# Kernel tuning notes

Measured on AMD Instinct MI355X. Metric: run time of the kernel, lower is better.

Reference implementation:

```python
import math
import jax, jax.numpy as jnp
import numpy as np

BS, N, D, H = 4, 512, 1024, 16
HD = D // H


def setup_inputs() -> dict:
    key = jax.random.key(0)
    ks = jax.random.split(key, 12)
    s = 1.0 / math.sqrt(D)
    return {
        "x": jax.random.normal(ks[0], (BS, N, D), jnp.float32),
        "r": jax.random.normal(ks[1], (BS, 3, N, N), jnp.float32),
        "bias": jax.random.normal(ks[2], (BS, H, N, N), jnp.float32),
        "mask": jax.random.randint(ks[3], (BS, 1, N, N), 0, 2, jnp.int32),
        "wq": jax.random.normal(ks[4], (D, D), jnp.float32) * s,
        "bq": jnp.zeros((D,), jnp.float32),
        "wk": jax.random.normal(ks[5], (D, D), jnp.float32) * s,
        "bk": jnp.zeros((D,), jnp.float32),
        "wv": jax.random.normal(ks[6], (D, D), jnp.float32) * s,
        "bv": jnp.zeros((D,), jnp.float32),
        "wo": jax.random.normal(ks[7], (D, 1), jnp.float32) * s,
        "bo": jnp.zeros((1,), jnp.float32),
    }


def reference(x, r, bias, mask, wq, bq, wk, bk, wv, bv, wo, bo):
    bs, n, d = x.shape
    # projections -> (bs, h, n, hd)
    q = (x @ wq + bq).reshape(bs, n, H, HD).transpose(0, 2, 1, 3)
    k = (x @ wk + bk).reshape(bs, n, H, HD).transpose(0, 2, 1, 3)
    v = (x @ wv + bv).reshape(bs, n, H, HD).transpose(0, 2, 1, 3)
    logits = jnp.einsum("bhid,bhjd->bhij", q, k) / math.sqrt(HD) + bias
    logits = jnp.where(mask == 0, jnp.float32(-1e9), logits)
    w = jax.nn.softmax(logits, axis=-1)  # (bs,h,n,n)
    # o[b,i,c,h,d] = sum_j r[b,c,i,j] * w[b,h,i,j] * v[b,h,j,d]
    o = jnp.einsum("bcij,bhij,bhjd->bichd", r, w, v)
    o = o.reshape(bs, n, 3, d)
    force = o @ wo + bo  # (bs, n, 3, 1)
    return force
```

## Files before the change

kernel.cpp:

```cpp
#include <hip/hip_runtime.h>
#include <stdint.h>

#define BSZ 4
#define NSEQ 512
#define DMOD 1024
#define NH 16
#define HD 64

typedef __attribute__((ext_vector_type(8))) short bf16x8;
typedef __attribute__((ext_vector_type(4))) float f32x4;

__device__ __forceinline__ unsigned short f2bf(float f) {
    union { float f; uint32_t u; } v; v.f = f;
    uint32_t u = v.u;
    u += 0x7FFFu + ((u >> 16) & 1u);
    return (unsigned short)(u >> 16);
}

__device__ __forceinline__ void gload_lds16(const unsigned short* g, unsigned short* l) {
    __builtin_amdgcn_global_load_lds(
        (const __attribute__((address_space(1))) void*)g,
        (__attribute__((address_space(3))) void*)l, 16, 0, 0);
}

__global__ __launch_bounds__(256) void k_prep(
        const float* __restrict__ x, const float* __restrict__ wq, const float* __restrict__ wk,
        const float* __restrict__ wv, const float* __restrict__ bv, const float* __restrict__ wo,
        unsigned short* __restrict__ xb, unsigned short* __restrict__ wqt,
        unsigned short* __restrict__ wkt, float* __restrict__ wv2t, float* __restrict__ bv2) {
    __shared__ float t[32][33];
    int bx = blockIdx.x, tid = threadIdx.x;
    if (bx < 2048) {
        int i = bx * 256 + tid;
        float4 v = ((const float4*)x)[i];
        ushort4 o; o.x = f2bf(v.x); o.y = f2bf(v.y); o.z = f2bf(v.z); o.w = f2bf(v.w);
        ((ushort4*)xb)[i] = o;
    } else if (bx < 4096) {
        int g = bx - 2048; int z = g >> 10; g &= 1023;
        const float* src = z ? wk : wq;
        unsigned short* dst = z ? wkt : wqt;
        int be = (g & 31) * 32, bc = (g >> 5) * 32;
        int tx = tid & 31, ty = tid >> 5;
        #pragma unroll
        for (int yy = 0; yy < 32; yy += 8)
            t[ty + yy][tx] = src[(size_t)(be + ty + yy) * DMOD + bc + tx];
        __syncthreads();
        #pragma unroll
        for (int yy = 0; yy < 32; yy += 8)
            dst[(size_t)(bc + ty + yy) * DMOD + be + tx] = f2bf(t[tx][ty + yy]);
    } else {
        int g = bx - 4096;
        int grp = tid >> 6, l = tid & 63;
        int e = g * 4 + grp;
        float out = 0.f;
        #pragma unroll
        for (int it = 0; it < 16; ++it) {
            float v = wv[(size_t)e * DMOD + it * 64 + l] * wo[it * 64 + l];
            #pragma unroll
            for (int off = 1; off < 64; off <<= 1) v += __shfl_xor(v, off, 64);
            if (l == it) out = v;
        }
        if (l < 16) wv2t[l * DMOD + e] = out;
        if (g == 0 && grp == 0) {
            float ob = 0.f;
            #pragma unroll
            for (int it = 0; it < 16; ++it) {
                float v = bv[it * 64 + l] * wo[it * 64 + l];
                #pragma unroll
                for (int off = 1; off < 64; off <<= 1) v += __shfl_xor(v, off, 64);
                if (l == it) ob = v;
            }
            if (l < 16) bv2[l] = ob;
        }
    }
}

__global__ __launch_bounds__(256, 3) void k_mid(
        const float* __restrict__ x, const float* __restrict__ wv2t, const float* __restrict__ bv2,
        const unsigned short* __restrict__ xb, const unsigned short* __restrict__ wqt,
        const unsigned short* __restrict__ wkt, const float* __restrict__ bq,
        const float* __restrict__ bk, float* __restrict__ u,
        unsigned short* __restrict__ qT, unsigned short* __restrict__ kT) {
    __shared__ unsigned short lA[128 * 64];
    __shared__ unsigned short lB[128 * 64];
    int bx = blockIdx.x, tid = threadIdx.x;
    if (bx >= 256) {
        int wave = (bx - 256) * 4 + (tid >> 6);
        int l = tid & 63;
        int b = wave >> 9, j = wave & 511;
        const float* xr = x + (size_t)(b * NSEQ + j) * DMOD;
        float p[16];
        #pragma unroll
        for (int h = 0; h < 16; ++h) p[h] = 0.f;
        for (int it = 0; it < 16; ++it) {
            int e = l + it * 64;
            float xv = xr[e];
            #pragma unroll
            for (int h = 0; h < 16; ++h) p[h] += xv * wv2t[h * DMOD + e];
        }
        #pragma unroll
        for (int h = 0; h < 16; ++h) {
            #pragma unroll
            for (int off = 1; off < 64; off <<= 1) p[h] += __shfl_xor(p[h], off, 64);
        }
        float out = 0.f;
        #pragma unroll
        for (int h = 0; h < 16; ++h) if (l == h) out = p[h] + bv2[h];
        if (l < 16) u[(b * 16 + l) * NSEQ + j] = out;
        return;
    }
    int g = bx;
    int mt = g & 15, nt8 = (g >> 4) & 7, z = g >> 7;
    const unsigned short* Wt = z ? wkt : wqt;
    const float* bias = z ? bk : bq;
    unsigned short* outT = z ? kT : qT;
    float scale = z ? 1.f : 0.125f;
    int m0 = mt * 128, n0 = nt8 * 128;
    int w = tid >> 6, lane = tid & 63;
    int wr = w >> 1, wc = w & 1;
    int quad = lane >> 4, cs = lane & 15;
    int l8 = lane >> 3, l7 = lane & 7;
    int sg = l7 ^ l8;

    f32x4 acc[4][4];
    #pragma unroll
    for (int mi = 0; mi < 4; ++mi)
        #pragma unroll
        for (int ni = 0; ni < 4; ++ni) acc[mi][ni] = (f32x4){0.f, 0.f, 0.f, 0.f};

    for (int kc = 0; kc < 16; ++kc) {
        int k0 = kc * 64;
        #pragma unroll
        for (int q = 0; q < 4; ++q) {
            int row = w * 32 + q * 8 + l8;
            gload_lds16(xb + (size_t)(m0 + row) * DMOD + k0 + sg * 8,
                        &lA[(w * 32 + q * 8) * 64]);
            gload_lds16(Wt + (size_t)(n0 + row) * DMOD + k0 + sg * 8,
                        &lB[(w * 32 + q * 8) * 64]);
        }
        __syncthreads();
        #pragma unroll
        for (int ks = 0; ks < 2; ++ks) {
            bf16x8 af[4], bfr[4];
            #pragma unroll
            for (int mi = 0; mi < 4; ++mi) {
                int row = wr * 64 + mi * 16 + cs;
                int gq = (ks * 4 + quad) ^ (row & 7);
                af[mi] = *(const bf16x8*)&lA[row * 64 + gq * 8];
            }
            #pragma unroll
            for (int ni = 0; ni < 4; ++ni) {
                int row = wc * 64 + ni * 16 + cs;
                int gq = (ks * 4 + quad) ^ (row & 7);
                bfr[ni] = *(const bf16x8*)&lB[row * 64 + gq * 8];
            }
            #pragma unroll
            for (int mi = 0; mi < 4; ++mi)
                #pragma unroll
                for (int ni = 0; ni < 4; ++ni)
                    acc[mi][ni] = __builtin_amdgcn_mfma_f32_16x16x32_bf16(
                        af[mi], bfr[ni], acc[mi][ni], 0, 0, 0);
        }
        __syncthreads();
    }
    #pragma unroll
    for (int ni = 0; ni < 4; ++ni) {
        int n = n0 + wc * 64 + ni * 16 + cs;
        int h = n >> 6, d = n & 63;
        float bvv = bias[n];
        #pragma unroll
        for (int mi = 0; mi < 4; ++mi) {
            #pragma unroll
            for (int rr = 0; rr < 4; ++rr) {
                int mg = m0 + wr * 64 + mi * 16 + quad * 4 + rr;
                int b = mg >> 9, i = mg & 511;
                outT[(size_t)((b * 16 + h) * NSEQ + i) * HD + d] =
                    f2bf((acc[mi][ni][rr] + bvv) * scale);
            }
        }
    }
}

__global__ __launch_bounds__(512, 4) void k_attn(
        const unsigned short* __restrict__ qT, const unsigned short* __restrict__ kT,
        const float* __restrict__ bias, const int* __restrict__ mask,
        const float* __restrict__ u, const float* __restrict__ r,
        float* __restrict__ spart, float* __restrict__ P) {
    __shared__ float rT4[16 * 64 * 4];
    int tid = threadIdx.x;
    int w = tid >> 6, lane = tid & 63;
    int quad = lane >> 4, col = lane & 15;
    int it = blockIdx.x, jc = blockIdx.y, bz = blockIdx.z;
    int b = bz >> 1, hg = bz & 1;
    int i0 = it * 16, j0 = jc * 64;
    int h = hg * 8 + w;
    int bh = b * 16 + h;

    float sr0[2], sr1[2], sr2[2], smf[2];
    const float* rbase = r + (size_t)b * 3 * NSEQ * NSEQ;
    const int* mrow = mask + (size_t)b * NSEQ * NSEQ;
    #pragma unroll
    for (int t = 0; t < 2; ++t) {
        int slot = t * 512 + tid;
        int il = slot >> 6, jl = slot & 63;
        size_t off = (size_t)(i0 + il) * NSEQ + j0 + jl;
        sr0[t] = rbase[off];
        sr1[t] = rbase[(size_t)NSEQ * NSEQ + off];
        sr2[t] = rbase[2 * (size_t)NSEQ * NSEQ + off];
        smf[t] = (float)mrow[off];
    }

    const unsigned short* qbase = qT + ((size_t)(bh * NSEQ + i0 + col)) * HD + quad * 8;
    bf16x8 a0 = *(const bf16x8*)qbase;
    bf16x8 a1 = *(const bf16x8*)(qbase + 32);

    bf16x8 kf0[4], kf1[4];
    #pragma unroll
    for (int jt = 0; jt < 4; ++jt) {
        const unsigned short* kbase = kT + ((size_t)(bh * NSEQ + j0 + jt * 16 + col)) * HD + quad * 8;
        kf0[jt] = *(const bf16x8*)kbase;
        kf1[jt] = *(const bf16x8*)(kbase + 32);
    }
    const float* brow = bias + (size_t)bh * NSEQ * NSEQ;
    float bvv[16];
    #pragma unroll
    for (int jt = 0; jt < 4; ++jt) {
        int j = j0 + jt * 16 + col;
        #pragma unroll
        for (int rr = 0; rr < 4; ++rr) {
            int i = i0 + quad * 4 + rr;
            bvv[jt * 4 + rr] = __builtin_nontemporal_load(&brow[(size_t)i * NSEQ + j]);
        }
    }
    const float* ub = u + (size_t)bh * NSEQ;
    float uvv[4];
    #pragma unroll
    for (int jt = 0; jt < 4; ++jt) uvv[jt] = ub[j0 + jt * 16 + col];

    #pragma unroll
    for (int t = 0; t < 2; ++t) {
        int slot = t * 512 + tid;
        float4 pk; pk.x = sr0[t]; pk.y = sr1[t]; pk.z = sr2[t]; pk.w = smf[t];
        *(float4*)&rT4[slot * 4] = pk;
    }

    asm volatile("s_waitcnt lgkmcnt(0)" ::: "memory");
    __builtin_amdgcn_sched_barrier(0);
    __builtin_amdgcn_s_barrier();
    __builtin_amdgcn_sched_barrier(0);

    float sp[4] = {0.f, 0.f, 0.f, 0.f};
    float pc0[4] = {0.f, 0.f, 0.f, 0.f};
    float pc1[4] = {0.f, 0.f, 0.f, 0.f};
    float pc2[4] = {0.f, 0.f, 0.f, 0.f};
    #pragma unroll
    for (int jt = 0; jt < 4; ++jt) {
        f32x4 acc = (f32x4){0.f, 0.f, 0.f, 0.f};
        acc = __builtin_amdgcn_mfma_f32_16x16x32_bf16(a0, kf0[jt], acc, 0, 0, 0);
        acc = __builtin_amdgcn_mfma_f32_16x16x32_bf16(a1, kf1[jt], acc, 0, 0, 0);
        float uv = uvv[jt];
        int jl = jt * 16 + col;
        #pragma unroll
        for (int rr = 0; rr < 4; ++rr) {
            int il = quad * 4 + rr;
            float4 v = *(const float4*)&rT4[(il * 64 + jl) * 4];
            float lg = acc[rr] + bvv[jt * 4 + rr];
            float e = __expf(lg) * v.w;
            sp[rr] += e;
            float eu = e * uv;
            pc0[rr] += eu * v.x;
            pc1[rr] += eu * v.y;
            pc2[rr] += eu * v.z;
        }
    }
    #pragma unroll
    for (int rr = 0; rr < 4; ++rr) {
        #pragma unroll
        for (int off = 1; off < 16; off <<= 1) {
            sp[rr]  += __shfl_xor(sp[rr], off, 64);
            pc0[rr] += __shfl_xor(pc0[rr], off, 64);
            pc1[rr] += __shfl_xor(pc1[rr], off, 64);
            pc2[rr] += __shfl_xor(pc2[rr], off, 64);
        }
    }
    if (col == 0) {
        #pragma unroll
        for (int rr = 0; rr < 4; ++rr) {
            int il = quad * 4 + rr;
            spart[((size_t)bh * NSEQ + i0 + il) * 8 + jc] = sp[rr];
            size_t pb = ((((size_t)bh * 32 + it) * 16 + il) * 8 + jc) * 3;
            P[pb + 0] = pc0[rr];
            P[pb + 1] = pc1[rr];
            P[pb + 2] = pc2[rr];
        }
    }
}

__global__ __launch_bounds__(256) void k_final(
        const float* __restrict__ spart, const float* __restrict__ P,
        const float* __restrict__ bo, float* __restrict__ out) {
    __shared__ float part[4][16][3];
    int bx = blockIdx.x;
    int b = bx >> 5, it = bx & 31;
    int tid = threadIdx.x;
    int il = tid & 15, h = tid >> 4;
    int w = tid >> 6;
    int bh = b * 16 + h;
    int i = it * 16 + il;
    const float* sprow = spart + ((size_t)bh * NSEQ + i) * 8;
    float4 sa = *(const float4*)sprow;
    float4 sb = *(const float4*)(sprow + 4);
    float s = sa.x + sa.y + sa.z + sa.w + sb.x + sb.y + sb.z + sb.w;
    float sinv = (s > 0.f) ? 1.f / s : 0.f;
    const float* pbase = P + (((size_t)bh * 32 + it) * 16 + il) * 24;
    float f[3] = {0.f, 0.f, 0.f};
    #pragma unroll
    for (int q = 0; q < 6; ++q) {
        float4 v = *(const float4*)(pbase + q * 4);
        f[(q * 4 + 0) % 3] += v.x;
        f[(q * 4 + 1) % 3] += v.y;
        f[(q * 4 + 2) % 3] += v.z;
        f[(q * 4 + 3) % 3] += v.w;
    }
    f[0] *= sinv; f[1] *= sinv; f[2] *= sinv;
    #pragma unroll
    for (int c = 0; c < 3; ++c) {
        f[c] += __shfl_xor(f[c], 16, 64);
        f[c] += __shfl_xor(f[c], 32, 64);
    }
    if ((tid & 48) == 0) {
        part[w][il][0] = f[0]; part[w][il][1] = f[1]; part[w][il][2] = f[2];
    }
    __syncthreads();
    if (tid < 16) {
        float bov = bo[0];
        float o0 = part[0][tid][0] + part[1][tid][0] + part[2][tid][0] + part[3][tid][0];
        float o1 = part[0][tid][1] + part[1][tid][1] + part[2][tid][1] + part[3][tid][1];
        float o2 = part[0][tid][2] + part[1][tid][2] + part[2][tid][2] + part[3][tid][2];
        size_t row = (size_t)b * NSEQ + it * 16 + tid;
        out[row * 3 + 0] = o0 + bov;
        out[row * 3 + 1] = o1 + bov;
        out[row * 3 + 2] = o2 + bov;
    }
}

extern "C" void kernel_launch(void* const* d_in, const int* in_sizes, int n_in,
                              void* d_out, int out_size, void* d_ws, size_t ws_size,
                              hipStream_t stream) {
    const float* x    = (const float*)d_in[0];
    const float* rr   = (const float*)d_in[1];
    const float* bias = (const float*)d_in[2];
    const int*   mask = (const int*)d_in[3];
    const float* wq   = (const float*)d_in[4];
    const float* bq   = (const float*)d_in[5];
    const float* wk   = (const float*)d_in[6];
    const float* bk   = (const float*)d_in[7];
    const float* wv   = (const float*)d_in[8];
    const float* bv   = (const float*)d_in[9];
    const float* wo   = (const float*)d_in[10];
    const float* bo   = (const float*)d_in[11];
    float* out = (float*)d_out;

    char* ws = (char*)d_ws;
    unsigned short* xb    = (unsigned short*)(ws + 0);
    unsigned short* wqt   = (unsigned short*)(ws + 4194304);
    unsigned short* wkt   = (unsigned short*)(ws + 6291456);
    float*          wv2t  = (float*)(ws + 8388608);
    float*          bv2   = (float*)(ws + 8454144);
    float*          u     = (float*)(ws + 8454400);
    unsigned short* qT    = (unsigned short*)(ws + 8585472);
    unsigned short* kT    = (unsigned short*)(ws + 12779776);
    float*          spart = (float*)(ws + 16974080);
    float*          P     = (float*)(ws + 18022656);

    k_prep<<<4352, 256, 0, stream>>>(x, wq, wk, wv, bv, wo, xb, wqt, wkt, wv2t, bv2);
    k_mid<<<768, 256, 0, stream>>>(x, wv2t, bv2, xb, wqt, wkt, bq, bk, u, qT, kT);
    k_attn<<<dim3(32, 8, 8), 512, 0, stream>>>(qT, kT, bias, mask, u, rr, spart, P);
    k_final<<<128, 256, 0, stream>>>(spart, P, bo, out);
}
```

Measured before the change: 191.1 us.

## Restructure attention grid per (batch,head) row block with LDS-staged bias

```diff
diff --git a/kernel.cpp b/kernel.cpp
--- a/kernel.cpp
+++ b/kernel.cpp
@@ -18,6 +18,12 @@
 }
 
 __device__ __forceinline__ void gload_lds16(const unsigned short* g, unsigned short* l) {
+    __builtin_amdgcn_global_load_lds(
+        (const __attribute__((address_space(1))) void*)g,
+        (__attribute__((address_space(3))) void*)l, 16, 0, 0);
+}
+
+__device__ __forceinline__ void gload_lds16f(const float* g, float* l) {
     __builtin_amdgcn_global_load_lds(
         (const __attribute__((address_space(1))) void*)g,
         (__attribute__((address_space(3))) void*)l, 16, 0, 0);
@@ -181,117 +187,116 @@
     }
 }
 
-__global__ __launch_bounds__(512, 4) void k_attn(
+#define BROW 516
+__global__ __launch_bounds__(256) void k_attn(
         const unsigned short* __restrict__ qT, const unsigned short* __restrict__ kT,
         const float* __restrict__ bias, const int* __restrict__ mask,
         const float* __restrict__ u, const float* __restrict__ r,
         float* __restrict__ spart, float* __restrict__ P) {
-    __shared__ float rT4[16 * 64 * 4];
+    __shared__ float blds[16 * BROW];
     int tid = threadIdx.x;
     int w = tid >> 6, lane = tid & 63;
     int quad = lane >> 4, col = lane & 15;
-    int it = blockIdx.x, jc = blockIdx.y, bz = blockIdx.z;
-    int b = bz >> 1, hg = bz & 1;
-    int i0 = it * 16, j0 = jc * 64;
-    int h = hg * 8 + w;
-    int bh = b * 16 + h;
-
-    float sr0[2], sr1[2], sr2[2], smf[2];
-    const float* rbase = r + (size_t)b * 3 * NSEQ * NSEQ;
-    const int* mrow = mask + (size_t)b * NSEQ * NSEQ;
-    #pragma unroll
-    for (int t = 0; t < 2; ++t) {
-        int slot = t * 512 + tid;
-        int il = slot >> 6, jl = slot & 63;
-        size_t off = (size_t)(i0 + il) * NSEQ + j0 + jl;
-        sr0[t] = rbase[off];
-        sr1[t] = rbase[(size_t)NSEQ * NSEQ + off];
-        sr2[t] = rbase[2 * (size_t)NSEQ * NSEQ + off];
-        smf[t] = (float)mrow[off];
+    int it = blockIdx.x, bh = blockIdx.y;
+    int b = bh >> 4;
+    int i0 = it * 16;
+
+    {
+        const float* browf = bias + ((size_t)bh * NSEQ + i0) * NSEQ;
+        #pragma unroll
+        for (int i = 0; i < 8; ++i) {
+            int c = i * 4 + w;
+            int row = c >> 1, half = c & 1;
+            gload_lds16f(browf + row * NSEQ + half * 256 + lane * 4,
+                         &blds[row * BROW + half * 256]);
+        }
     }
 
     const unsigned short* qbase = qT + ((size_t)(bh * NSEQ + i0 + col)) * HD + quad * 8;
     bf16x8 a0 = *(const bf16x8*)qbase;
     bf16x8 a1 = *(const bf16x8*)(qbase + 32);
 
-    bf16x8 kf0[4], kf1[4];
-    #pragma unroll
-    for (int jt = 0; jt < 4; ++jt) {
-        const unsigned short* kbase = kT + ((size_t)(bh * NSEQ + j0 + jt * 16 + col)) * HD + quad * 8;
-        kf0[jt] = *(const bf16x8*)kbase;
-        kf1[jt] = *(const bf16x8*)(kbase + 32);
-    }
-    const float* brow = bias + (size_t)bh * NSEQ * NSEQ;
-    float bvv[16];
-    #pragma unroll
-    for (int jt = 0; jt < 4; ++jt) {
-        int j = j0 + jt * 16 + col;
+    const float* rbase = r + (size_t)b * 3 * NSEQ * NSEQ;
+    const int* mrow = mask + (size_t)b * NSEQ * NSEQ;
+    const unsigned short* kbh = kT + (size_t)bh * NSEQ * HD;
+    const float* ub = u + (size_t)bh * NSEQ;
+
+    __syncthreads();
+
+    #pragma unroll
+    for (int s = 0; s < 2; ++s) {
+        int jc = w * 2 + s;
+        int j0 = jc * 64;
+
+        bf16x8 kf0[4], kf1[4];
+        float uvv[4];
+        #pragma unroll
+        for (int jt = 0; jt < 4; ++jt) {
+            const unsigned short* kb = kbh + ((size_t)(j0 + jt * 16 + col)) * HD + quad * 8;
+            kf0[jt] = *(const bf16x8*)kb;
+            kf1[jt] = *(const bf16x8*)(kb + 32);
+            uvv[jt] = ub[j0 + jt * 16 + col];
+        }
+        float rv0[16], rv1[16], rv2[16];
+        int mv[16];
+        #pragma unroll
+        for (int jt = 0; jt < 4; ++jt) {
+            int j = j0 + jt * 16 + col;
+            #pragma unroll
+            for (int rr = 0; rr < 4; ++rr) {
+                int i = i0 + quad * 4 + rr;
+                size_t off = (size_t)i * NSEQ + j;
+                rv0[jt * 4 + rr] = rbase[off];
+                rv1[jt * 4 + rr] = rbase[(size_t)NSEQ * NSEQ + off];
+                rv2[jt * 4 + rr] = rbase[2 * (size_t)NSEQ * NSEQ + off];
+                mv[jt * 4 + rr] = mrow[off];
+            }
+        }
+
+        float sp[4]  = {0.f, 0.f, 0.f, 0.f};
+        float pc0[4] = {0.f, 0.f, 0.f, 0.f};
+        float pc1[4] = {0.f, 0.f, 0.f, 0.f};
+        float pc2[4] = {0.f, 0.f, 0.f, 0.f};
+        #pragma unroll
+        for (int jt = 0; jt < 4; ++jt) {
+            f32x4 acc = (f32x4){0.f, 0.f, 0.f, 0.f};
+            acc = __builtin_amdgcn_mfma_f32_16x16x32_bf16(a0, kf0[jt], acc, 0, 0, 0);
+            acc = __builtin_amdgcn_mfma_f32_16x16x32_bf16(a1, kf1[jt], acc, 0, 0, 0);
+            float uv = uvv[jt];
+            int jl = j0 + jt * 16 + col;
+            #pragma unroll
+            for (int rr = 0; rr < 4; ++rr) {
+                int il = quad * 4 + rr;
+                float bvv = blds[il * BROW + jl];
+                float lg = acc[rr] + bvv;
+                float e = (mv[jt * 4 + rr] == 0) ? 0.f : __expf(lg);
+                sp[rr] += e;
+                float eu = e * uv;
+                pc0[rr] += eu * rv0[jt * 4 + rr];
+                pc1[rr] += eu * rv1[jt * 4 + rr];
+                pc2[rr] += eu * rv2[jt * 4 + rr];
+            }
+        }
         #pragma unroll
         for (int rr = 0; rr < 4; ++rr) {
-            int i = i0 + quad * 4 + rr;
-            bvv[jt * 4 + rr] = __builtin_nontemporal_load(&brow[(size_t)i * NSEQ + j]);
-        }
-    }
-    const float* ub = u + (size_t)bh * NSEQ;
-    float uvv[4];
-    #pragma unroll
-    for (int jt = 0; jt < 4; ++jt) uvv[jt] = ub[j0 + jt * 16 + col];
-
-    #pragma unroll
-    for (int t = 0; t < 2; ++t) {
-        int slot = t * 512 + tid;
-        float4 pk; pk.x = sr0[t]; pk.y = sr1[t]; pk.z = sr2[t]; pk.w = smf[t];
-        *(float4*)&rT4[slot * 4] = pk;
-    }
-
-    asm volatile("s_waitcnt lgkmcnt(0)" ::: "memory");
-    __builtin_amdgcn_sched_barrier(0);
-    __builtin_amdgcn_s_barrier();
-    __builtin_amdgcn_sched_barrier(0);
-
-    float sp[4] = {0.f, 0.f, 0.f, 0.f};
-    float pc0[4] = {0.f, 0.f, 0.f, 0.f};
-    float pc1[4] = {0.f, 0.f, 0.f, 0.f};
-    float pc2[4] = {0.f, 0.f, 0.f, 0.f};
-    #pragma unroll
-    for (int jt = 0; jt < 4; ++jt) {
-        f32x4 acc = (f32x4){0.f, 0.f, 0.f, 0.f};
-        acc = __builtin_amdgcn_mfma_f32_16x16x32_bf16(a0, kf0[jt], acc, 0, 0, 0);
-        acc = __builtin_amdgcn_mfma_f32_16x16x32_bf16(a1, kf1[jt], acc, 0, 0, 0);
-        float uv = uvv[jt];
-        int jl = jt * 16 + col;
-        #pragma unroll
-        for (int rr = 0; rr < 4; ++rr) {
-            int il = quad * 4 + rr;
-            float4 v = *(const float4*)&rT4[(il * 64 + jl) * 4];
-            float lg = acc[rr] + bvv[jt * 4 + rr];
-            float e = __expf(lg) * v.w;
-            sp[rr] += e;
-            float eu = e * uv;
-            pc0[rr] += eu * v.x;
-            pc1[rr] += eu * v.y;
-            pc2[rr] += eu * v.z;
-        }
-    }
-    #pragma unroll
-    for (int rr = 0; rr < 4; ++rr) {
-        #pragma unroll
-        for (int off = 1; off < 16; off <<= 1) {
-            sp[rr]  += __shfl_xor(sp[rr], off, 64);
-            pc0[rr] += __shfl_xor(pc0[rr], off, 64);
-            pc1[rr] += __shfl_xor(pc1[rr], off, 64);
-            pc2[rr] += __shfl_xor(pc2[rr], off, 64);
-        }
-    }
-    if (col == 0) {
-        #pragma unroll
-        for (int rr = 0; rr < 4; ++rr) {
-            int il = quad * 4 + rr;
-            spart[((size_t)bh * NSEQ + i0 + il) * 8 + jc] = sp[rr];
-            size_t pb = ((((size_t)bh * 32 + it) * 16 + il) * 8 + jc) * 3;
-            P[pb + 0] = pc0[rr];
-            P[pb + 1] = pc1[rr];
-            P[pb + 2] = pc2[rr];
+            #pragma unroll
+            for (int off = 1; off < 16; off <<= 1) {
+                sp[rr]  += __shfl_xor(sp[rr], off, 64);
+                pc0[rr] += __shfl_xor(pc0[rr], off, 64);
+                pc1[rr] += __shfl_xor(pc1[rr], off, 64);
+                pc2[rr] += __shfl_xor(pc2[rr], off, 64);
+            }
+        }
+        if (col == 0) {
+            #pragma unroll
+            for (int rr = 0; rr < 4; ++rr) {
+                int il = quad * 4 + rr;
+                spart[((size_t)bh * NSEQ + i0 + il) * 8 + jc] = sp[rr];
+                size_t pb2 = ((((size_t)bh * 32 + it) * 16 + il) * 8 + jc) * 3;
+                P[pb2 + 0] = pc0[rr];
+                P[pb2 + 1] = pc1[rr];
+                P[pb2 + 2] = pc2[rr];
+            }
         }
     }
 }
@@ -375,6 +380,6 @@
 
     k_prep<<<4352, 256, 0, stream>>>(x, wq, wk, wv, bv, wo, xb, wqt, wkt, wv2t, bv2);
     k_mid<<<768, 256, 0, stream>>>(x, wv2t, bv2, xb, wqt, wkt, bq, bk, u, qT, kT);
-    k_attn<<<dim3(32, 8, 8), 512, 0, stream>>>(qT, kT, bias, mask, u, rr, spart, P);
+    k_attn<<<dim3(32, 64), 256, 0, stream>>>(qT, kT, bias, mask, u, rr, spart, P);
     k_final<<<128, 256, 0, stream>>>(spart, P, bo, out);
 }
```

Result: slower. 197.3 us (+3.2%).
